# Performance work log

Measured on AMD Instinct MI355X. Metric: run time of the kernel, lower is better.

## Reference

```python
import jax, jax.numpy as jnp
import numpy as np

B, S, H, F, K = 32, 512, 256, 256, 3
NBINS, MAX_MEL = 256, 2048


def _conv1d(x, w, b):
    # x: [B,S,Cin], w: [K,Cin,Cout] -> [B,S,Cout], padding 1 (SAME, k=3)
    return jax.lax.conv_general_dilated(x, w, (1,), 'SAME',
        dimension_numbers=('NWC', 'WIO', 'NWC')) + b


def _ln(x, g, b):
    m = jnp.mean(x, -1, keepdims=True)
    v = jnp.var(x, -1, keepdims=True)
    return (x - m) * jax.lax.rsqrt(v + 1e-5) * g + b


def _predictor(x, mask, p):
    # FastSpeech2 VariancePredictor (eval mode, dropout off)
    w1, b1, g1, be1, w2, b2, g2, be2, wl, bl = p
    h = _ln(jax.nn.relu(_conv1d(x, w1, b1)), g1, be1)
    h = _ln(jax.nn.relu(_conv1d(h, w2, b2)), g2, be2)
    out = (h @ wl + bl)[..., 0]  # [B,S]
    return jnp.where(mask, 0.0, out)  # masked_fill(mask, 0.0)


def _make_predictor_params(key, out_bias):
    ks = jax.random.split(key, 3)
    w1 = jax.random.normal(ks[0], (K, H, F), jnp.float32) * 0.03
    w2 = jax.random.normal(ks[1], (K, F, F), jnp.float32) * 0.03
    wl = jax.random.normal(ks[2], (F, 1), jnp.float32) * 0.02
    return [w1, jnp.zeros((F,), jnp.float32), jnp.ones((F,), jnp.float32), jnp.zeros((F,), jnp.float32),
            w2, jnp.zeros((F,), jnp.float32), jnp.ones((F,), jnp.float32), jnp.zeros((F,), jnp.float32),
            wl, jnp.full((1,), out_bias, jnp.float32)]


PNAMES = ['w1', 'b1', 'g1', 'be1', 'w2', 'b2', 'g2', 'be2', 'wl', 'bl']


def setup_inputs() -> dict:
    key = jax.random.key(0)
    ks = jax.random.split(key, 8)
    inp = {
        'x': jax.random.normal(ks[0], (B, S, H), jnp.float32),
        'src_mask': jnp.zeros((B, S), jnp.bool_),  # True = padded position
        'pitch_control': jnp.float32(1.0),
        'energy_control': jnp.float32(1.0),
        'duration_control': jnp.float32(1.0),
        'pitch_bins': jnp.linspace(-4.0, 4.0, NBINS - 1, dtype=jnp.float32),
        'energy_bins': jnp.linspace(-4.0, 4.0, NBINS - 1, dtype=jnp.float32),
        'pitch_emb': jax.random.normal(ks[1], (NBINS, H), jnp.float32) * 0.02,
        'energy_emb': jax.random.normal(ks[2], (NBINS, H), jnp.float32) * 0.02,
    }
    # duration predictor output bias 1.6 ~ log(5) -> avg ~4 frames/phoneme
    for i, (pref, ob) in enumerate([('dur', 1.6), ('pit', 0.0), ('ene', 0.0)]):
        for n, v in zip(PNAMES, _make_predictor_params(ks[3 + i], ob)):
            inp[pref + '_' + n] = v
    return inp


def reference(x, src_mask, pitch_control, energy_control, duration_control,
              pitch_bins, energy_bins, pitch_emb, energy_emb,
              dur_w1, dur_b1, dur_g1, dur_be1, dur_w2, dur_b2, dur_g2, dur_be2, dur_wl, dur_bl,
              pit_w1, pit_b1, pit_g1, pit_be1, pit_w2, pit_b2, pit_g2, pit_be2, pit_wl, pit_bl,
              ene_w1, ene_b1, ene_g1, ene_be1, ene_w2, ene_b2, ene_g2, ene_be2, ene_wl, ene_bl):
    dur_p = [dur_w1, dur_b1, dur_g1, dur_be1, dur_w2, dur_b2, dur_g2, dur_be2, dur_wl, dur_bl]
    pit_p = [pit_w1, pit_b1, pit_g1, pit_be1, pit_w2, pit_b2, pit_g2, pit_be2, pit_wl, pit_bl]
    ene_p = [ene_w1, ene_b1, ene_g1, ene_be1, ene_w2, ene_b2, ene_g2, ene_be2, ene_wl, ene_bl]

    log_dur = _predictor(x, src_mask, dur_p)                      # [B,S]
    pitch_pred = _predictor(x, src_mask, pit_p) * pitch_control   # inference: scaled prediction
    # torch.bucketize(v, bins) (right=False) == searchsorted side='left'
    x = x + pitch_emb[jnp.searchsorted(pitch_bins, pitch_pred, side='left')]
    energy_pred = _predictor(x, src_mask, ene_p) * energy_control
    x = x + energy_emb[jnp.searchsorted(energy_bins, energy_pred, side='left')]

    dur = jnp.maximum(jnp.round(jnp.exp(log_dur) - 1.0) * duration_control, 0.0)  # [B,S]
    dur_i = dur.astype(jnp.int32)
    mel_len = jnp.minimum(jnp.sum(dur_i, -1), MAX_MEL)            # [B]
    # Length regulator: frame t maps to phoneme idx = #{cumdur <= t}
    cum = jnp.cumsum(dur_i, 1)                                    # [B,S]
    t = jnp.arange(MAX_MEL, dtype=jnp.int32)
    idx = jax.vmap(lambda c: jnp.searchsorted(c, t, side='right'))(cum)  # [B,MAX_MEL]
    idx = jnp.clip(idx, 0, S - 1)
    x_exp = jnp.take_along_axis(x, idx[:, :, None], axis=1)       # [B,MAX_MEL,H]
    mel_mask = t[None, :] >= mel_len[:, None]                     # True = padded frame
    x_exp = jnp.where(mel_mask[:, :, None], 0.0, x_exp)
    return (x_exp, pitch_pred, energy_pred, log_dur, dur, mel_len, mel_mask)
```

## Files before the change

### kernel.cpp

```cpp
#include <hip/hip_runtime.h>
#include <stdint.h>

#define BB 32
#define SS 512
#define HH 256
#define MM (BB*SS)
#define MAXMEL 2048

typedef _Float16 f16;
typedef _Float16 f16x4 __attribute__((ext_vector_type(4)));
typedef _Float16 f16x8 __attribute__((ext_vector_type(8)));
typedef float    f32x16 __attribute__((ext_vector_type(16)));

#define BAR()  asm volatile("s_barrier" ::: "memory")
#define VMW0() asm volatile("s_waitcnt vmcnt(0)" ::: "memory")

__device__ __forceinline__ size_t xoff(int row, int chan) {
  int cb = chan >> 4, g = (chan >> 3) & 1, e = chan & 7;
  int rp = row >> 1, par = row & 1;
  int slot = (2 * par + g) ^ ((rp >> 1) & 3);
  return (((size_t)cb * (MM / 2) + rp) * 4 + slot) * 8 + e;
}

#define BOFF  0
#define AOFF  24576
#define AZ    32768
#define LDSSZ 32832
#define WSZ   ((size_t)768 * 256)

__global__ __launch_bounds__(256, 4) void conv64(
    const f16* __restrict__ X0h, const f16* __restrict__ X0l,
    const f16* __restrict__ X1h_, const f16* __restrict__ X1l_,
    const f16* __restrict__ W0h, const f16* __restrict__ W0l,
    const f16* __restrict__ W1h, const f16* __restrict__ W1l,
    const float* __restrict__ bias0, const float* __restrict__ bias1,
    f16* __restrict__ Y0h, f16* __restrict__ Y0l,
    f16* __restrict__ Y1h, f16* __restrict__ Y1l)
{
  __shared__ __align__(16) unsigned char smem[LDSSZ];
  const int tid = threadIdx.x;
  const int lane = tid & 63, wid = tid >> 6;
  const int bm = blockIdx.x, bn = blockIdx.y, bz = blockIdx.z;
  const int l31 = lane & 31, half = lane >> 5;
  const int hx4 = half << 4;
  const int wr = wid >> 1, wc = wid & 1;

  const f16* Xh = bz ? X1h_ : X0h;
  const f16* Xl = bz ? X1l_ : X0l;
  const f16* Wh = bz ? W1h : W0h;
  const f16* Wl = bz ? W1l : W0l;

  const f16* sb[8]; int sdst[8];
  size_t sstr;
  #pragma unroll
  for (int i = 0; i < 8; ++i) {
    int j = wid * 8 + i;
    if (j < 8) {
      int p = j >> 2, seg = j & 3;
      int rowstart = bm * 64 - 32 + seg * 32;
      rowstart = rowstart < 0 ? 0 : (rowstart > MM - 32 ? MM - 32 : rowstart);
      sb[i]   = (p ? Xl : Xh) + (size_t)(rowstart >> 1) * 32 + lane * 8;
      sdst[i] = AOFF + p * 4096 + seg * 1024 + lane * 16;
    } else {
      int jj = j - 8;
      int tap = jj >> 3, rem = jj & 7;
      int p = rem >> 2, q4 = rem & 3;
      sb[i]   = (p ? Wl : Wh) + ((size_t)((bn * 16) * 3 + tap) * 256 + q4 * 64 + lane) * 8;
      sdst[i] = tap * 8192 + p * 4096 + q4 * 1024 + lane * 16;
    }
  }
  sstr = (wid == 0) ? (size_t)(MM / 2) * 32 : (size_t)3 * 256 * 8;

  int a_addr[3][2];
  #pragma unroll
  for (int tap = 0; tap < 3; ++tap) {
    int row_l = wr * 32 + l31;
    int sseq = (bm & 7) * 64 + row_l + tap - 1;
    bool valid = (unsigned)sseq < 512u;
    int lrow = row_l + tap + 31;
    int rp = lrow >> 1, par = lrow & 1;
    int slot0 = (2 * par) ^ ((rp >> 1) & 3);
    int base = AOFF + rp * 64 + slot0 * 16;
    a_addr[tap][0] = valid ? base : AZ;
    a_addr[tap][1] = valid ? (base + 4096) : AZ;
  }
  int b_base[2];
  #pragma unroll
  for (int n = 0; n < 2; ++n) {
    int col = wc * 64 + n * 32 + l31;
    int cp = col >> 1, cpar = col & 1;
    int slot0 = (2 * cpar) ^ ((cp >> 1) & 3);
    b_base[n] = cp * 64 + slot0 * 16;
  }

  f32x16 acc[2];
  acc[0] = (f32x16)0.f;
  acc[1] = (f32x16)0.f;

  auto STAGE = [&](int step) {
    #pragma unroll
    for (int i = 0; i < 8; ++i)
      __builtin_amdgcn_global_load_lds(
        (const __attribute__((address_space(1))) void*)(sb[i] + (size_t)step * sstr),
        (__attribute__((address_space(3))) void*)(smem + sdst[i]), 16, 0, 0);
  };

  auto COMP = [&]() {
    #pragma unroll
    for (int tap = 0; tap < 3; ++tap) {
      f16x8 av[2], bv[2][2];
      #pragma unroll
      for (int p = 0; p < 2; ++p) {
        av[p] = *(const f16x8*)(smem + (a_addr[tap][p] ^ hx4));
        #pragma unroll
        for (int n = 0; n < 2; ++n)
          bv[p][n] = *(const f16x8*)(smem + (tap * 8192 + p * 4096 + (b_base[n] ^ hx4)));
      }
      #pragma unroll
      for (int n = 0; n < 2; ++n) {
        acc[n] = __builtin_amdgcn_mfma_f32_32x32x16_f16(av[0], bv[0][n], acc[n], 0, 0, 0);
        acc[n] = __builtin_amdgcn_mfma_f32_32x32x16_f16(av[0], bv[1][n], acc[n], 0, 0, 0);
        acc[n] = __builtin_amdgcn_mfma_f32_32x32x16_f16(av[1], bv[0][n], acc[n], 0, 0, 0);
      }
    }
  };

  if (tid < 4)
    *(float4*)(smem + AZ + tid * 16) = make_float4(0.f, 0.f, 0.f, 0.f);
  STAGE(0);
  __syncthreads();

  for (int i = 0; i < 16; ++i) {
    COMP();
    if (i < 15) {
      BAR();
      STAGE(i + 1);
      VMW0();
      BAR();
    }
  }

  const float* bias = bz ? bias1 : bias0;
  f16* Yh = bz ? Y1h : Y0h;
  f16* Yl = bz ? Y1l : Y0l;
  #pragma unroll
  for (int n = 0; n < 2; ++n) {
    int colg = bn * 128 + wc * 64 + n * 32 + l31;
    float bvs = bias[colg];
    int cb = colg >> 4, g = (colg >> 3) & 1, e = colg & 7;
    #pragma unroll
    for (int r = 0; r < 16; ++r) {
      int rowl = (r & 3) + 8 * (r >> 2) + 4 * half;
      int rowg = bm * 64 + wr * 32 + rowl;
      float v = fmaxf(acc[n][r] + bvs, 0.f);
      f16 h = (f16)v;
      f16 l = (f16)(v - (float)h);
      int rp = rowg >> 1, par = rowg & 1;
      int slot = (2 * par + g) ^ ((rp >> 1) & 3);
      size_t o = (((size_t)cb * (MM / 2) + rp) * 4 + slot) * 8 + e;
      Yh[o] = h;
      Yl[o] = l;
    }
  }
}

__global__ __launch_bounds__(256) void wsplit6(
    const float* __restrict__ W0, const float* __restrict__ W1,
    const float* __restrict__ W2, const float* __restrict__ W3,
    const float* __restrict__ W4, const float* __restrict__ W5,
    f16* __restrict__ Wt)
{
  int z = blockIdx.y;
  const float* W = z==0?W0 : z==1?W1 : z==2?W2 : z==3?W3 : z==4?W4 : W5;
  f16* Thi = Wt + (size_t)z * 2 * WSZ;
  f16* Tlo = Thi + WSZ;
  int id = blockIdx.x * 256 + threadIdx.x;
  int slot = id & 3, cp = (id >> 2) & 63;
  int t3 = id >> 8;
  int tap = t3 % 3, bs = t3 / 3;
  int step = bs & 15, bnn = bs >> 4;
  int s2 = slot ^ ((cp >> 1) & 3);
  int cpar = s2 >> 1, g = s2 & 1;
  int col = cp * 2 + cpar;
  int chan = step * 16 + g * 8;
  int colg = bnn * 128 + col;
  f16x8 hi, lo;
  #pragma unroll
  for (int e = 0; e < 8; ++e) {
    float w = W[(size_t)(tap * 256 + chan + e) * 256 + colg];
    f16 h = (f16)w;
    hi[e] = h;
    lo[e] = (f16)(w - (float)h);
  }
  *(f16x8*)(Thi + (size_t)id * 8) = hi;
  *(f16x8*)(Tlo + (size_t)id * 8) = lo;
}

__global__ __launch_bounds__(256) void split2(
    const float* __restrict__ X, f16* __restrict__ Hi, f16* __restrict__ Lo)
{
  int id = blockIdx.x * 256 + threadIdx.x;
  int row = id >> 5, chan = (id & 31) * 8;
  const float* src = X + (size_t)row * 256 + chan;
  float4 v0 = *(const float4*)src;
  float4 v1 = *(const float4*)(src + 4);
  float vv[8] = {v0.x, v0.y, v0.z, v0.w, v1.x, v1.y, v1.z, v1.w};
  f16x8 h, l;
  #pragma unroll
  for (int j = 0; j < 8; ++j) {
    f16 hh = (f16)vv[j];
    h[j] = hh;
    l[j] = (f16)(vv[j] - (float)hh);
  }
  size_t o = xoff(row, chan);
  *(f16x8*)(Hi + o) = h;
  *(f16x8*)(Lo + o) = l;
}

__global__ __launch_bounds__(256) void lnF(
    f16* __restrict__ P0h, f16* __restrict__ P0l,
    f16* __restrict__ P1h, f16* __restrict__ P1l,
    const float* __restrict__ g0, const float* __restrict__ be0,
    const float* __restrict__ g1, const float* __restrict__ be1)
{
  int z = blockIdx.y;
  f16* Ph = z ? P1h : P0h;
  f16* Pl = z ? P1l : P0l;
  const float* g  = z ? g1 : g0;
  const float* be = z ? be1 : be0;
  int row  = blockIdx.x * 4 + (threadIdx.x >> 6);
  int lane = threadIdx.x & 63;
  size_t o = xoff(row, lane * 4);
  f16x4 h = *(const f16x4*)(Ph + o);
  f16x4 l = *(const f16x4*)(Pl + o);
  float v[4];
  #pragma unroll
  for (int j = 0; j < 4; ++j) v[j] = (float)h[j] + (float)l[j];
  float s = v[0] + v[1] + v[2] + v[3];
  float q = v[0]*v[0] + v[1]*v[1] + v[2]*v[2] + v[3]*v[3];
  #pragma unroll
  for (int d = 32; d > 0; d >>= 1) { s += __shfl_xor(s, d); q += __shfl_xor(q, d); }
  float mean = s * (1.f / 256.f);
  float var  = q * (1.f / 256.f) - mean * mean;
  float inv  = 1.0f / sqrtf(var + 1e-5f);
  float4 gg = *(const float4*)(g + lane * 4);
  float4 bb = *(const float4*)(be + lane * 4);
  float gv[4] = {gg.x, gg.y, gg.z, gg.w};
  float bv[4] = {bb.x, bb.y, bb.z, bb.w};
  #pragma unroll
  for (int j = 0; j < 4; ++j) {
    float oo = (v[j] - mean) * inv * gv[j] + bv[j];
    f16 hh = (f16)oo;
    h[j] = hh;
    l[j] = (f16)(oo - (float)hh);
  }
  *(f16x4*)(Ph + o) = h;
  *(f16x4*)(Pl + o) = l;
}

__global__ __launch_bounds__(256) void lnheadD(
    const f16* __restrict__ U0h, const f16* __restrict__ U0l,
    const f16* __restrict__ U1h, const f16* __restrict__ U1l,
    const float* __restrict__ g0, const float* __restrict__ be0,
    const float* __restrict__ wl0, const float* __restrict__ bl0,
    const float* __restrict__ g1, const float* __restrict__ be1,
    const float* __restrict__ wl1, const float* __restrict__ bl1,
    const unsigned char* __restrict__ mask, const float* __restrict__ pc,
    float* __restrict__ o_ldur, float* __restrict__ pred_d,
    float* __restrict__ o_pit,
    const float* __restrict__ pbins, const float* __restrict__ pemb,
    const f16* __restrict__ XPh, const f16* __restrict__ XPl,
    f16* __restrict__ X1h, f16* __restrict__ X1l)
{
  int z = blockIdx.y;
  int row  = blockIdx.x * 4 + (threadIdx.x >> 6);
  int lane = threadIdx.x & 63;
  size_t o = xoff(row, lane * 4);
  const f16* Uh = z ? U1h : U0h;
  const f16* Ul = z ? U1l : U0l;
  f16x4 h = *(const f16x4*)(Uh + o);
  f16x4 l = *(const f16x4*)(Ul + o);
  float v[4];
  #pragma unroll
  for (int j = 0; j < 4; ++j) v[j] = (float)h[j] + (float)l[j];
  float s = v[0] + v[1] + v[2] + v[3];
  float q = v[0]*v[0] + v[1]*v[1] + v[2]*v[2] + v[3]*v[3];
  #pragma unroll
  for (int d = 32; d > 0; d >>= 1) { s += __shfl_xor(s, d); q += __shfl_xor(q, d); }
  float mean = s * (1.f / 256.f);
  float var  = q * (1.f / 256.f) - mean * mean;
  float inv  = 1.0f / sqrtf(var + 1e-5f);
  const float* g  = z ? g1  : g0;
  const float* be = z ? be1 : be0;
  const float* wl = z ? wl1 : wl0;
  float4 gg = *(const float4*)(g + lane * 4);
  float4 bb = *(const float4*)(be + lane * 4);
  float4 ww = *(const float4*)(wl + lane * 4);
  float gv[4] = {gg.x, gg.y, gg.z, gg.w};
  float bv[4] = {bb.x, bb.y, bb.z, bb.w};
  float wv[4] = {ww.x, ww.y, ww.z, ww.w};
  float acc = 0.f;
  #pragma unroll
  for (int j = 0; j < 4; ++j)
    acc += ((v[j] - mean) * inv * gv[j] + bv[j]) * wv[j];
  #pragma unroll
  for (int d = 32; d > 0; d >>= 1) acc += __shfl_xor(acc, d);
  float r = acc + (z ? bl1 : bl0)[0];
  if (mask[row]) r = 0.f;
  if (z == 0) {
    if (lane == 0) { o_ldur[row] = r; pred_d[row] = r; }
  } else {
    r *= pc[0];
    if (lane == 0) o_pit[row] = r;
    int lo = 0, hi = 255;
    while (lo < hi) { int mid = (lo + hi) >> 1; if (pbins[mid] < r) lo = mid + 1; else hi = mid; }
    f16x4 xh = *(const f16x4*)(XPh + o);
    f16x4 xl = *(const f16x4*)(XPl + o);
    float4 e = *(const float4*)(pemb + (size_t)lo * HH + lane * 4);
    float ev[4] = {e.x, e.y, e.z, e.w};
    #pragma unroll
    for (int j = 0; j < 4; ++j) {
      float oo = (float)xh[j] + (float)xl[j] + ev[j];
      f16 hh = (f16)oo;
      xh[j] = hh;
      xl[j] = (f16)(oo - (float)hh);
    }
    *(f16x4*)(X1h + o) = xh;
    *(f16x4*)(X1l + o) = xl;
  }
}

__global__ __launch_bounds__(256) void lnheadE(
    const f16* __restrict__ Uh, const f16* __restrict__ Ul,
    const float* __restrict__ g, const float* __restrict__ be,
    const float* __restrict__ wl, const float* __restrict__ bl,
    const unsigned char* __restrict__ mask, const float* __restrict__ ec,
    float* __restrict__ o_ene,
    const float* __restrict__ ebins, const float* __restrict__ eemb,
    const f16* __restrict__ X1h, const f16* __restrict__ X1l,
    f16* __restrict__ X2h, f16* __restrict__ X2l)
{
  int row  = blockIdx.x * 4 + (threadIdx.x >> 6);
  int lane = threadIdx.x & 63;
  size_t o = xoff(row, lane * 4);
  f16x4 h = *(const f16x4*)(Uh + o);
  f16x4 l = *(const f16x4*)(Ul + o);
  float v[4];
  #pragma unroll
  for (int j = 0; j < 4; ++j) v[j] = (float)h[j] + (float)l[j];
  float s = v[0] + v[1] + v[2] + v[3];
  float q = v[0]*v[0] + v[1]*v[1] + v[2]*v[2] + v[3]*v[3];
  #pragma unroll
  for (int d = 32; d > 0; d >>= 1) { s += __shfl_xor(s, d); q += __shfl_xor(q, d); }
  float mean = s * (1.f / 256.f);
  float var  = q * (1.f / 256.f) - mean * mean;
  float inv  = 1.0f / sqrtf(var + 1e-5f);
  float4 gg = *(const float4*)(g + lane * 4);
  float4 bb = *(const float4*)(be + lane * 4);
  float4 ww = *(const float4*)(wl + lane * 4);
  float gv[4] = {gg.x, gg.y, gg.z, gg.w};
  float bv[4] = {bb.x, bb.y, bb.z, bb.w};
  float wv[4] = {ww.x, ww.y, ww.z, ww.w};
  float acc = 0.f;
  #pragma unroll
  for (int j = 0; j < 4; ++j)
    acc += ((v[j] - mean) * inv * gv[j] + bv[j]) * wv[j];
  #pragma unroll
  for (int d = 32; d > 0; d >>= 1) acc += __shfl_xor(acc, d);
  float r = acc + bl[0];
  if (mask[row]) r = 0.f;
  r *= ec[0];
  if (lane == 0) o_ene[row] = r;
  int lo = 0, hi = 255;
  while (lo < hi) { int mid = (lo + hi) >> 1; if (ebins[mid] < r) lo = mid + 1; else hi = mid; }
  f16x4 xh = *(const f16x4*)(X1h + o);
  f16x4 xl = *(const f16x4*)(X1l + o);
  float4 e = *(const float4*)(eemb + (size_t)lo * HH + lane * 4);
  float ev[4] = {e.x, e.y, e.z, e.w};
  #pragma unroll
  for (int j = 0; j < 4; ++j) {
    float oo = (float)xh[j] + (float)xl[j] + ev[j];
    f16 hh = (f16)oo;
    xh[j] = hh;
    xl[j] = (f16)(oo - (float)hh);
  }
  *(f16x4*)(X2h + o) = xh;
  *(f16x4*)(X2l + o) = xl;
}

__global__ __launch_bounds__(512) void dur_post(
    const float* __restrict__ logdur, const float* __restrict__ dc,
    float* __restrict__ out_dur, float* __restrict__ out_mel_len,
    int* __restrict__ cum_ws, int* __restrict__ mel_len_ws)
{
  __shared__ int wsum[8];
  int b = blockIdx.x, t = threadIdx.x;
  float ld = logdur[b * SS + t];
  float d  = fmaxf(rintf(expf(ld) - 1.f) * dc[0], 0.f);
  out_dur[b * SS + t] = d;
  int di = (int)d;
  int lane = t & 63, w = t >> 6;
  int x = di;
  #pragma unroll
  for (int dd = 1; dd < 64; dd <<= 1) {
    int n = __shfl_up(x, dd);
    if (lane >= dd) x += n;
  }
  if (lane == 63) wsum[w] = x;
  __syncthreads();
  int off = 0;
  for (int i = 0; i < w; ++i) off += wsum[i];
  x += off;
  cum_ws[b * SS + t] = x;
  if (t == SS - 1) {
    int ml = min(x, MAXMEL);
    mel_len_ws[b] = ml;
    out_mel_len[b] = (float)ml;
  }
}

__global__ __launch_bounds__(256) void gather_planes(
    const f16* __restrict__ Xhi, const f16* __restrict__ Xlo,
    const int* __restrict__ cum, const int* __restrict__ mel_len_ws,
    float* __restrict__ out_x, float* __restrict__ out_mask)
{
  __shared__ int c[SS];
  int b   = blockIdx.y;
  int tid = threadIdx.x;
  c[tid]       = cum[b * SS + tid];
  c[tid + 256] = cum[b * SS + tid + 256];
  __syncthreads();
  int w = tid >> 6, lane = tid & 63;
  int t = blockIdx.x * 4 + w;
  int lo = 0, hi = SS;
  while (lo < hi) { int mid = (lo + hi) >> 1; if (c[mid] <= t) lo = mid + 1; else hi = mid; }
  int idx = min(lo, SS - 1);
  int ml  = mel_len_ws[b];
  bool m  = (t >= ml);
  float4 v = make_float4(0.f, 0.f, 0.f, 0.f);
  if (!m) {
    size_t o = xoff(b * SS + idx, lane * 4);
    f16x4 xh = *(const f16x4*)(Xhi + o);
    f16x4 xl = *(const f16x4*)(Xlo + o);
    v.x = (float)xh[0] + (float)xl[0];
    v.y = (float)xh[1] + (float)xl[1];
    v.z = (float)xh[2] + (float)xl[2];
    v.w = (float)xh[3] + (float)xl[3];
  }
  *(float4*)(out_x + ((size_t)b * MAXMEL + t) * HH + lane * 4) = v;
  if (lane == 0) out_mask[b * MAXMEL + t] = m ? 1.f : 0.f;
}

extern "C" void kernel_launch(void* const* d_in, const int* in_sizes, int n_in,
                              void* d_out, int out_size, void* d_ws, size_t ws_size,
                              hipStream_t stream) {
  const float* x     = (const float*)d_in[0];
  const unsigned char* smask = (const unsigned char*)d_in[1];
  const float* pc    = (const float*)d_in[2];
  const float* ec    = (const float*)d_in[3];
  const float* dc    = (const float*)d_in[4];
  const float* pbins = (const float*)d_in[5];
  const float* ebins = (const float*)d_in[6];
  const float* pemb  = (const float*)d_in[7];
  const float* eemb  = (const float*)d_in[8];

  float* out = (float*)d_out;
  float* o_xexp  = out;
  float* o_pit   = out + (size_t)16777216;
  float* o_ene   = o_pit + 16384;
  float* o_ldur  = o_ene + 16384;
  float* o_dur   = o_ldur + 16384;
  float* o_mlen  = o_dur + 16384;
  float* o_mmask = o_mlen + 32;

  const size_t PL = (size_t)MM * HH;
  f16* p = (f16*)d_ws;
  f16 *XPh = p,        *XPl = p + PL;
  f16 *Tdh = p + 2*PL, *Tdl = p + 3*PL;
  f16 *Tph = p + 4*PL, *Tpl = p + 5*PL;
  f16 *Udh = p + 6*PL, *Udl = p + 7*PL;
  f16 *Uph = p + 8*PL, *Upl = p + 9*PL;
  f16 *X1h = p + 10*PL, *X1l = p + 11*PL;
  f16 *Teh = p + 12*PL, *Tel = p + 13*PL;
  f16 *Ueh = p + 14*PL, *Uel = p + 15*PL;
  f16 *X2h = p + 16*PL, *X2l = p + 17*PL;
  f16* Wt  = p + 18*PL;
  float* pred_d = (float*)(Wt + 12 * WSZ);
  int*   cum = (int*)(pred_d + MM);
  int*   mlw = cum + MM;

  #define WPH(i) (Wt + (size_t)(i) * 2 * WSZ)
  #define WPL(i) (Wt + (size_t)(i) * 2 * WSZ + WSZ)

  wsplit6<<<dim3(96, 6), 256, 0, stream>>>(
      (const float*)d_in[9], (const float*)d_in[13], (const float*)d_in[19],
      (const float*)d_in[23], (const float*)d_in[29], (const float*)d_in[33], Wt);

  split2<<<2048, 256, 0, stream>>>(x, XPh, XPl);

  dim3 cgrid2(256, 2, 2);
  dim3 cgrid1(256, 2, 1);
  dim3 rgrid(MM / 4);
  dim3 rgrid2(MM / 4, 2);

  conv64<<<cgrid2, 256, 0, stream>>>(
      XPh, XPl, XPh, XPl,
      WPH(0), WPL(0), WPH(2), WPL(2),
      (const float*)d_in[10], (const float*)d_in[20],
      Tdh, Tdl, Tph, Tpl);
  lnF<<<rgrid2, 256, 0, stream>>>(Tdh, Tdl, Tph, Tpl,
      (const float*)d_in[11], (const float*)d_in[12],
      (const float*)d_in[21], (const float*)d_in[22]);
  conv64<<<cgrid2, 256, 0, stream>>>(
      Tdh, Tdl, Tph, Tpl,
      WPH(1), WPL(1), WPH(3), WPL(3),
      (const float*)d_in[14], (const float*)d_in[24],
      Udh, Udl, Uph, Upl);
  lnheadD<<<rgrid2, 256, 0, stream>>>(
      Udh, Udl, Uph, Upl,
      (const float*)d_in[15], (const float*)d_in[16],
      (const float*)d_in[17], (const float*)d_in[18],
      (const float*)d_in[25], (const float*)d_in[26],
      (const float*)d_in[27], (const float*)d_in[28],
      smask, pc, o_ldur, pred_d, o_pit, pbins, pemb,
      XPh, XPl, X1h, X1l);
  dur_post<<<BB, 512, 0, stream>>>(pred_d, dc, o_dur, o_mlen, cum, mlw);

  conv64<<<cgrid1, 256, 0, stream>>>(
      X1h, X1l, X1h, X1l,
      WPH(4), WPL(4), WPH(4), WPL(4),
      (const float*)d_in[30], (const float*)d_in[30],
      Teh, Tel, Teh, Tel);
  lnF<<<dim3(MM / 4, 1), 256, 0, stream>>>(Teh, Tel, Teh, Tel,
      (const float*)d_in[31], (const float*)d_in[32],
      (const float*)d_in[31], (const float*)d_in[32]);
  conv64<<<cgrid1, 256, 0, stream>>>(
      Teh, Tel, Teh, Tel,
      WPH(5), WPL(5), WPH(5), WPL(5),
      (const float*)d_in[34], (const float*)d_in[34],
      Ueh, Uel, Ueh, Uel);
  lnheadE<<<rgrid, 256, 0, stream>>>(Ueh, Uel,
      (const float*)d_in[35], (const float*)d_in[36],
      (const float*)d_in[37], (const float*)d_in[38],
      smask, ec, o_ene, ebins, eemb, X1h, X1l, X2h, X2l);

  dim3 ggrid(MAXMEL / 4, BB);
  gather_planes<<<ggrid, 256, 0, stream>>>(X2h, X2l, cum, mlw, o_xexp, o_mmask);

  #undef WPH
  #undef WPL
}
```

Before: 248.1 us.

## Replace LDS-staged conv GEMM with direct global-to-register MFMA loads and bigger tiles

Rewrites the conv kernel to drop LDS staging and barriers, loading A and B fragments directly from global memory into registers each K-step. Doubles the per-block M tile to 128 rows, with each wave computing a 2x2 grid of 32x32 MFMA tiles. Activations move to a simpler channel-block-major layout, and the weights are packed hi/lo interleaved to match. It removes barrier and LDS-copy overhead but relies on L1/L2 for reuse, adds register pressure, and may raise global load traffic.

Measured after the change: 301.7 us. 1.22x slower.

```diff
diff --git a/kernel.cpp b/kernel.cpp
--- a/kernel.cpp
+++ b/kernel.cpp
@@ -12,156 +12,124 @@
 typedef _Float16 f16x8 __attribute__((ext_vector_type(8)));
 typedef float    f32x16 __attribute__((ext_vector_type(16)));
 
-#define BAR()  asm volatile("s_barrier" ::: "memory")
-#define VMW0() asm volatile("s_waitcnt vmcnt(0)" ::: "memory")
-
 __device__ __forceinline__ size_t xoff(int row, int chan) {
-  int cb = chan >> 4, g = (chan >> 3) & 1, e = chan & 7;
-  int rp = row >> 1, par = row & 1;
-  int slot = (2 * par + g) ^ ((rp >> 1) & 3);
-  return (((size_t)cb * (MM / 2) + rp) * 4 + slot) * 8 + e;
-}
-
-#define BOFF  0
-#define AOFF  24576
-#define AZ    32768
-#define LDSSZ 32832
-#define WSZ   ((size_t)768 * 256)
-
-__global__ __launch_bounds__(256, 4) void conv64(
+  return ((size_t)(chan >> 4) * MM + row) * 16 + (chan & 15);
+}
+
+#define WSZP ((size_t)393216)
+
+__global__ __launch_bounds__(256) void convA(
     const f16* __restrict__ X0h, const f16* __restrict__ X0l,
     const f16* __restrict__ X1h_, const f16* __restrict__ X1l_,
-    const f16* __restrict__ W0h, const f16* __restrict__ W0l,
-    const f16* __restrict__ W1h, const f16* __restrict__ W1l,
+    const f16* __restrict__ W0,  const f16* __restrict__ W1,
     const float* __restrict__ bias0, const float* __restrict__ bias1,
     f16* __restrict__ Y0h, f16* __restrict__ Y0l,
     f16* __restrict__ Y1h, f16* __restrict__ Y1l)
 {
-  __shared__ __align__(16) unsigned char smem[LDSSZ];
   const int tid = threadIdx.x;
   const int lane = tid & 63, wid = tid >> 6;
   const int bm = blockIdx.x, bn = blockIdx.y, bz = blockIdx.z;
   const int l31 = lane & 31, half = lane >> 5;
-  const int hx4 = half << 4;
   const int wr = wid >> 1, wc = wid & 1;
 
   const f16* Xh = bz ? X1h_ : X0h;
   const f16* Xl = bz ? X1l_ : X0l;
-  const f16* Wh = bz ? W1h : W0h;
-  const f16* Wl = bz ? W1l : W0l;
-
-  const f16* sb[8]; int sdst[8];
-  size_t sstr;
-  #pragma unroll
-  for (int i = 0; i < 8; ++i) {
-    int j = wid * 8 + i;
-    if (j < 8) {
-      int p = j >> 2, seg = j & 3;
-      int rowstart = bm * 64 - 32 + seg * 32;
-      rowstart = rowstart < 0 ? 0 : (rowstart > MM - 32 ? MM - 32 : rowstart);
-      sb[i]   = (p ? Xl : Xh) + (size_t)(rowstart >> 1) * 32 + lane * 8;
-      sdst[i] = AOFF + p * 4096 + seg * 1024 + lane * 16;
-    } else {
-      int jj = j - 8;
-      int tap = jj >> 3, rem = jj & 7;
-      int p = rem >> 2, q4 = rem & 3;
-      sb[i]   = (p ? Wl : Wh) + ((size_t)((bn * 16) * 3 + tap) * 256 + q4 * 64 + lane) * 8;
-      sdst[i] = tap * 8192 + p * 4096 + q4 * 1024 + lane * 16;
+  const f16* Wp = bz ? W1 : W0;
+
+  const f16* aptr[2][3][2];
+  bool vld[2][3];
+  #pragma unroll
+  for (int mi = 0; mi < 2; ++mi)
+    #pragma unroll
+    for (int tap = 0; tap < 3; ++tap) {
+      int row_l = wr * 64 + mi * 32 + l31;
+      int sseq  = (bm & 3) * 128 + row_l + tap - 1;
+      vld[mi][tap] = ((unsigned)sseq < 512u);
+      int rowg = bm * 128 + row_l + tap - 1;
+      rowg = rowg < 0 ? 0 : (rowg >= MM ? MM - 1 : rowg);
+      size_t o = (size_t)rowg * 16 + half * 8;
+      aptr[mi][tap][0] = Xh + o;
+      aptr[mi][tap][1] = Xl + o;
     }
-  }
-  sstr = (wid == 0) ? (size_t)(MM / 2) * 32 : (size_t)3 * 256 * 8;
-
-  int a_addr[3][2];
-  #pragma unroll
-  for (int tap = 0; tap < 3; ++tap) {
-    int row_l = wr * 32 + l31;
-    int sseq = (bm & 7) * 64 + row_l + tap - 1;
-    bool valid = (unsigned)sseq < 512u;
-    int lrow = row_l + tap + 31;
-    int rp = lrow >> 1, par = lrow & 1;
-    int slot0 = (2 * par) ^ ((rp >> 1) & 3);
-    int base = AOFF + rp * 64 + slot0 * 16;
-    a_addr[tap][0] = valid ? base : AZ;
-    a_addr[tap][1] = valid ? (base + 4096) : AZ;
-  }
-  int b_base[2];
-  #pragma unroll
-  for (int n = 0; n < 2; ++n) {
-    int col = wc * 64 + n * 32 + l31;
-    int cp = col >> 1, cpar = col & 1;
-    int slot0 = (2 * cpar) ^ ((cp >> 1) & 3);
-    b_base[n] = cp * 64 + slot0 * 16;
-  }
-
-  f32x16 acc[2];
-  acc[0] = (f32x16)0.f;
-  acc[1] = (f32x16)0.f;
-
-  auto STAGE = [&](int step) {
-    #pragma unroll
-    for (int i = 0; i < 8; ++i)
-      __builtin_amdgcn_global_load_lds(
-        (const __attribute__((address_space(1))) void*)(sb[i] + (size_t)step * sstr),
-        (__attribute__((address_space(3))) void*)(smem + sdst[i]), 16, 0, 0);
-  };
-
-  auto COMP = [&]() {
-    #pragma unroll
-    for (int tap = 0; tap < 3; ++tap) {
-      f16x8 av[2], bv[2][2];
+
+  const f16* bptr[3][2][2];
+  #pragma unroll
+  for (int tap = 0; tap < 3; ++tap)
+    #pragma unroll
+    for (int p = 0; p < 2; ++p)
       #pragma unroll
-      for (int p = 0; p < 2; ++p) {
-        av[p] = *(const f16x8*)(smem + (a_addr[tap][p] ^ hx4));
+      for (int n = 0; n < 2; ++n) {
+        int col = wc * 64 + n * 32 + l31;
+        size_t u = ((((size_t)(bn * 16) * 2 + p) * 3 + tap) * 128 + col) * 16
+                   + half * 8;
+        bptr[tap][p][n] = Wp + u;
+      }
+
+  f32x16 acc[2][2];
+  #pragma unroll
+  for (int mi = 0; mi < 2; ++mi)
+    #pragma unroll
+    for (int ni = 0; ni < 2; ++ni) acc[mi][ni] = (f32x16)0.f;
+
+  const size_t astr = (size_t)MM * 16;
+  const size_t bstr = (size_t)12288;
+
+  #pragma unroll
+  for (int t = 0; t < 16; ++t) {
+    f16x8 av[2][3][2];
+    #pragma unroll
+    for (int mi = 0; mi < 2; ++mi)
+      #pragma unroll
+      for (int tap = 0; tap < 3; ++tap)
+        #pragma unroll
+        for (int p = 0; p < 2; ++p)
+          av[mi][tap][p] = *(const f16x8*)(aptr[mi][tap][p] + (size_t)t * astr);
+    if (!vld[0][0]) { av[0][0][0] = (f16x8)(f16)0.f; av[0][0][1] = (f16x8)(f16)0.f; }
+    if (!vld[1][2]) { av[1][2][0] = (f16x8)(f16)0.f; av[1][2][1] = (f16x8)(f16)0.f; }
+
+    f16x8 bv[3][2][2];
+    #pragma unroll
+    for (int tap = 0; tap < 3; ++tap)
+      #pragma unroll
+      for (int p = 0; p < 2; ++p)
         #pragma unroll
         for (int n = 0; n < 2; ++n)
-          bv[p][n] = *(const f16x8*)(smem + (tap * 8192 + p * 4096 + (b_base[n] ^ hx4)));
-      }
+          bv[tap][p][n] = *(const f16x8*)(bptr[tap][p][n] + (size_t)t * bstr);
+
+    #pragma unroll
+    for (int tap = 0; tap < 3; ++tap)
       #pragma unroll
-      for (int n = 0; n < 2; ++n) {
-        acc[n] = __builtin_amdgcn_mfma_f32_32x32x16_f16(av[0], bv[0][n], acc[n], 0, 0, 0);
-        acc[n] = __builtin_amdgcn_mfma_f32_32x32x16_f16(av[0], bv[1][n], acc[n], 0, 0, 0);
-        acc[n] = __builtin_amdgcn_mfma_f32_32x32x16_f16(av[1], bv[0][n], acc[n], 0, 0, 0);
-      }
-    }
-  };
-
-  if (tid < 4)
-    *(float4*)(smem + AZ + tid * 16) = make_float4(0.f, 0.f, 0.f, 0.f);
-  STAGE(0);
-  __syncthreads();
-
-  for (int i = 0; i < 16; ++i) {
-    COMP();
-    if (i < 15) {
-      BAR();
-      STAGE(i + 1);
-      VMW0();
-      BAR();
-    }
+      for (int mi = 0; mi < 2; ++mi)
+        #pragma unroll
+        for (int ni = 0; ni < 2; ++ni) {
+          acc[mi][ni] = __builtin_amdgcn_mfma_f32_32x32x16_f16(av[mi][tap][0], bv[tap][0][ni], acc[mi][ni], 0, 0, 0);
+          acc[mi][ni] = __builtin_amdgcn_mfma_f32_32x32x16_f16(av[mi][tap][0], bv[tap][1][ni], acc[mi][ni], 0, 0, 0);
+          acc[mi][ni] = __builtin_amdgcn_mfma_f32_32x32x16_f16(av[mi][tap][1], bv[tap][0][ni], acc[mi][ni], 0, 0, 0);
+        }
   }
 
   const float* bias = bz ? bias1 : bias0;
   f16* Yh = bz ? Y1h : Y0h;
   f16* Yl = bz ? Y1l : Y0l;
   #pragma unroll
-  for (int n = 0; n < 2; ++n) {
-    int colg = bn * 128 + wc * 64 + n * 32 + l31;
-    float bvs = bias[colg];
-    int cb = colg >> 4, g = (colg >> 3) & 1, e = colg & 7;
-    #pragma unroll
-    for (int r = 0; r < 16; ++r) {
-      int rowl = (r & 3) + 8 * (r >> 2) + 4 * half;
-      int rowg = bm * 64 + wr * 32 + rowl;
-      float v = fmaxf(acc[n][r] + bvs, 0.f);
-      f16 h = (f16)v;
-      f16 l = (f16)(v - (float)h);
-      int rp = rowg >> 1, par = rowg & 1;
-      int slot = (2 * par + g) ^ ((rp >> 1) & 3);
-      size_t o = (((size_t)cb * (MM / 2) + rp) * 4 + slot) * 8 + e;
-      Yh[o] = h;
-      Yl[o] = l;
+  for (int mi = 0; mi < 2; ++mi)
+    #pragma unroll
+    for (int ni = 0; ni < 2; ++ni) {
+      int colg = bn * 128 + wc * 64 + ni * 32 + l31;
+      float bvs = bias[colg];
+      size_t cbase = (size_t)(colg >> 4) * MM * 16 + (colg & 15);
+      #pragma unroll
+      for (int r = 0; r < 16; ++r) {
+        int rowl = (r & 3) + 8 * (r >> 2) + 4 * half;
+        int rowg = bm * 128 + wr * 64 + mi * 32 + rowl;
+        float v = fmaxf(acc[mi][ni][r] + bvs, 0.f);
+        f16 h = (f16)v;
+        f16 l = (f16)(v - (float)h);
+        size_t o = cbase + (size_t)rowg * 16;
+        Yh[o] = h;
+        Yl[o] = l;
+      }
     }
-  }
 }
 
 __global__ __launch_bounds__(256) void wsplit6(
@@ -172,28 +140,28 @@
 {
   int z = blockIdx.y;
   const float* W = z==0?W0 : z==1?W1 : z==2?W2 : z==3?W3 : z==4?W4 : W5;
-  f16* Thi = Wt + (size_t)z * 2 * WSZ;
-  f16* Tlo = Thi + WSZ;
+  f16* T = Wt + (size_t)z * WSZP;
   int id = blockIdx.x * 256 + threadIdx.x;
-  int slot = id & 3, cp = (id >> 2) & 63;
-  int t3 = id >> 8;
-  int tap = t3 % 3, bs = t3 / 3;
-  int step = bs & 15, bnn = bs >> 4;
-  int s2 = slot ^ ((cp >> 1) & 3);
-  int cpar = s2 >> 1, g = s2 & 1;
-  int col = cp * 2 + cpar;
-  int chan = step * 16 + g * 8;
-  int colg = bnn * 128 + col;
-  f16x8 hi, lo;
+  int g = id & 1;
+  int t1 = id >> 1;
+  int col = t1 & 127;
+  int t2 = t1 >> 7;
+  int tap = t2 % 3;
+  int t3 = t2 / 3;
+  int p = t3 & 1;
+  int t4 = t3 >> 1;
+  int s = t4 & 15;
+  int bn = t4 >> 4;
+  int chan = s * 16 + g * 8;
+  int colg = bn * 128 + col;
+  f16x8 o;
   #pragma unroll
   for (int e = 0; e < 8; ++e) {
     float w = W[(size_t)(tap * 256 + chan + e) * 256 + colg];
     f16 h = (f16)w;
-    hi[e] = h;
-    lo[e] = (f16)(w - (float)h);
-  }
-  *(f16x8*)(Thi + (size_t)id * 8) = hi;
-  *(f16x8*)(Tlo + (size_t)id * 8) = lo;
+    o[e] = p ? (f16)(w - (float)h) : h;
+  }
+  *(f16x8*)(T + (size_t)id * 8) = o;
 }
 
 __global__ __launch_bounds__(256) void split2(
@@ -485,35 +453,32 @@
   f16 *Ueh = p + 14*PL, *Uel = p + 15*PL;
   f16 *X2h = p + 16*PL, *X2l = p + 17*PL;
   f16* Wt  = p + 18*PL;
-  float* pred_d = (float*)(Wt + 12 * WSZ);
+  float* pred_d = (float*)(Wt + 6 * WSZP);
   int*   cum = (int*)(pred_d + MM);
   int*   mlw = cum + MM;
 
-  #define WPH(i) (Wt + (size_t)(i) * 2 * WSZ)
-  #define WPL(i) (Wt + (size_t)(i) * 2 * WSZ + WSZ)
-
-  wsplit6<<<dim3(96, 6), 256, 0, stream>>>(
+  #define WPK(i) (Wt + (size_t)(i) * WSZP)
+
+  wsplit6<<<dim3(192, 6), 256, 0, stream>>>(
       (const float*)d_in[9], (const float*)d_in[13], (const float*)d_in[19],
       (const float*)d_in[23], (const float*)d_in[29], (const float*)d_in[33], Wt);
 
   split2<<<2048, 256, 0, stream>>>(x, XPh, XPl);
 
-  dim3 cgrid2(256, 2, 2);
-  dim3 cgrid1(256, 2, 1);
+  dim3 cgrid2(128, 2, 2);
+  dim3 cgrid1(128, 2, 1);
   dim3 rgrid(MM / 4);
   dim3 rgrid2(MM / 4, 2);
 
-  conv64<<<cgrid2, 256, 0, stream>>>(
-      XPh, XPl, XPh, XPl,
-      WPH(0), WPL(0), WPH(2), WPL(2),
+  convA<<<cgrid2, 256, 0, stream>>>(
+      XPh, XPl, XPh, XPl, WPK(0), WPK(2),
       (const float*)d_in[10], (const float*)d_in[20],
       Tdh, Tdl, Tph, Tpl);
   lnF<<<rgrid2, 256, 0, stream>>>(Tdh, Tdl, Tph, Tpl,
       (const float*)d_in[11], (const float*)d_in[12],
       (const float*)d_in[21], (const float*)d_in[22]);
-  conv64<<<cgrid2, 256, 0, stream>>>(
-      Tdh, Tdl, Tph, Tpl,
-      WPH(1), WPL(1), WPH(3), WPL(3),
+  convA<<<cgrid2, 256, 0, stream>>>(
+      Tdh, Tdl, Tph, Tpl, WPK(1), WPK(3),
       (const float*)d_in[14], (const float*)d_in[24],
       Udh, Udl, Uph, Upl);
   lnheadD<<<rgrid2, 256, 0, stream>>>(
@@ -526,17 +491,15 @@
       XPh, XPl, X1h, X1l);
   dur_post<<<BB, 512, 0, stream>>>(pred_d, dc, o_dur, o_mlen, cum, mlw);
 
-  conv64<<<cgrid1, 256, 0, stream>>>(
-      X1h, X1l, X1h, X1l,
-      WPH(4), WPL(4), WPH(4), WPL(4),
+  convA<<<cgrid1, 256, 0, stream>>>(
+      X1h, X1l, X1h, X1l, WPK(4), WPK(4),
       (const float*)d_in[30], (const float*)d_in[30],
       Teh, Tel, Teh, Tel);
   lnF<<<dim3(MM / 4, 1), 256, 0, stream>>>(Teh, Tel, Teh, Tel,
       (const float*)d_in[31], (const float*)d_in[32],
       (const float*)d_in[31], (const float*)d_in[32]);
-  conv64<<<cgrid1, 256, 0, stream>>>(
-      Teh, Tel, Teh, Tel,
-      WPH(5), WPL(5), WPH(5), WPL(5),
+  convA<<<cgrid1, 256, 0, stream>>>(
+      Teh, Tel, Teh, Tel, WPK(5), WPK(5),
       (const float*)d_in[34], (const float*)d_in[34],
       Ueh, Uel, Ueh, Uel);
   lnheadE<<<rgrid, 256, 0, stream>>>(Ueh, Uel,
@@ -547,6 +510,5 @@
   dim3 ggrid(MAXMEL / 4, BB);
   gather_planes<<<ggrid, 256, 0, stream>>>(X2h, X2l, cum, mlw, o_xexp, o_mmask);
 
-  #undef WPH
-  #undef WPL
-}
+  #undef WPK
+}
```
